# Optimization experiments

Hardware: AMD Instinct MI355X
Metric: run time of the kernel (lower is better)

## Reference

```python
import jax, jax.numpy as jnp
import numpy as np

K = 5        # spline kernel_size per dim (dim=2 -> 25 weight slots)
N = 60000    # input nodes
E = 360000   # input edges
N1 = 30000   # nodes after first graclus/max_pool
E2 = 180000  # edges of pooled graph
N2 = 15000   # nodes after second graclus pooling
G = 60       # graphs in batch


def _spline_basis(pseudo):
    """Open B-spline basis, degree 1, dim 2. pseudo: [E,2] in [0,1].
    Returns flat weight indices [E,4] and basis products [E,4]."""
    v = pseudo * (K - 1)
    i0 = jnp.clip(jnp.floor(v).astype(jnp.int32), 0, K - 1)   # [E,2]
    frac = v - jnp.floor(v)                                   # [E,2]
    idxs, ws = [], []
    for s0 in (0, 1):
        for s1 in (0, 1):
            ix = jnp.clip(i0[:, 0] + s0, 0, K - 1)
            iy = jnp.clip(i0[:, 1] + s1, 0, K - 1)
            w0 = frac[:, 0] if s0 else 1.0 - frac[:, 0]
            w1 = frac[:, 1] if s1 else 1.0 - frac[:, 1]
            idxs.append(ix + K * iy)
            ws.append(w0 * w1)
    return jnp.stack(idxs, -1), jnp.stack(ws, -1)


def _spline_conv(x, edge_index, pseudo, W, root, bias, num_nodes):
    """SplineConv: B-spline weighted messages, mean aggregation, root weight + bias."""
    src, dst = edge_index[0], edge_index[1]
    e = src.shape[0]
    idx, b = _spline_basis(pseudo)
    # dense per-edge basis over 25 kernel slots (only 4 nonzero per edge)
    B = jnp.zeros((e, K * K), x.dtype).at[jnp.arange(e)[:, None], idx].add(b)
    x_j = x[src]                                   # [E,Fin]
    fin, fout = W.shape[1], W.shape[2]
    xb = B[:, :, None] * x_j[:, None, :]           # [E,25,Fin]
    msg = xb.reshape(e, K * K * fin) @ W.reshape(K * K * fin, fout)
    agg = jax.ops.segment_sum(msg, dst, num_segments=num_nodes)
    cnt = jax.ops.segment_sum(jnp.ones((e,), x.dtype), dst, num_segments=num_nodes)
    agg = agg / jnp.maximum(cnt, 1.0)[:, None]     # mean aggregation
    return agg + x @ root + bias


def _seg_max_f(x, seg, n):
    m = jax.ops.segment_max(x, seg, num_segments=n)
    cnt = jax.ops.segment_sum(jnp.ones(seg.shape, x.dtype), seg, num_segments=n)
    return jnp.where((cnt > 0)[:, None], m, 0.0)


def _seg_max_i(x, seg, n):
    m = jax.ops.segment_max(x, seg, num_segments=n)
    return jnp.maximum(m, 0)


def _cartesian(pos, edge_index):
    # T.Cartesian(cat=False): attr = (pos[col]-pos[row]) / (2*max|.|) + 0.5
    cart = pos[edge_index[1]] - pos[edge_index[0]]
    scale = jnp.maximum(jnp.max(jnp.abs(cart)), 1e-12)
    return cart / (2.0 * scale) + 0.5


def setup_inputs():
    key = jax.random.key(0)
    ks = jax.random.split(key, 18)
    return {
        'x': jax.random.normal(ks[0], (N, 1), jnp.float32),
        'pos': jax.random.uniform(ks[1], (N, 2), jnp.float32),
        'edge_attr': jax.random.uniform(ks[2], (E, 2), jnp.float32),
        'edge_index': jax.random.randint(ks[3], (2, E), 0, N, jnp.int32),
        'batch': jnp.sort(jax.random.randint(ks[4], (N,), 0, G, jnp.int32)),
        'cluster1': jax.random.randint(ks[5], (N,), 0, N1, jnp.int32),
        'edge_index2': jax.random.randint(ks[6], (2, E2), 0, N1, jnp.int32),
        'cluster2': jax.random.randint(ks[7], (N1,), 0, N2, jnp.int32),
        'W1': jax.random.normal(ks[8], (K * K, 1, 32), jnp.float32) * 0.1,
        'root1': jax.random.normal(ks[9], (1, 32), jnp.float32) * 0.1,
        'bias1': jnp.zeros((32,), jnp.float32),
        'W2': jax.random.normal(ks[10], (K * K, 32, 64), jnp.float32) * 0.05,
        'root2': jax.random.normal(ks[11], (32, 64), jnp.float32) * 0.05,
        'bias2': jnp.zeros((64,), jnp.float32),
        'fc1_w': jax.random.normal(ks[12], (64, 128), jnp.float32) * 0.05,
        'fc1_b': jnp.zeros((128,), jnp.float32),
        'fc2_w': jax.random.normal(ks[13], (128, 3), jnp.float32) * 0.05,
        'fc2_b': jnp.zeros((3,), jnp.float32),
    }


def reference(x, pos, edge_attr, edge_index, batch, cluster1, edge_index2,
              cluster2, W1, root1, bias1, W2, root2, bias2,
              fc1_w, fc1_b, fc2_w, fc2_b):
    # conv1 + elu
    h = jax.nn.elu(_spline_conv(x, edge_index, edge_attr, W1, root1, bias1, N))
    # max_pool over graclus cluster1 (cluster given as input), Cartesian edge attrs
    x1 = _seg_max_f(h, cluster1, N1)
    pcnt = jax.ops.segment_sum(jnp.ones((N,), pos.dtype), cluster1, num_segments=N1)
    pos1 = jax.ops.segment_sum(pos, cluster1, num_segments=N1) / jnp.maximum(pcnt, 1.0)[:, None]
    batch1 = _seg_max_i(batch, cluster1, N1)
    attr2 = _cartesian(pos1, edge_index2)
    # conv2 + elu
    h2 = jax.nn.elu(_spline_conv(x1, edge_index2, attr2, W2, root2, bias2, N1))
    # max_pool_x over cluster2
    x2 = _seg_max_f(h2, cluster2, N2)
    batch2 = _seg_max_i(batch1, cluster2, N2)
    # global mean pool over graphs
    gsum = jax.ops.segment_sum(x2, batch2, num_segments=G)
    gcnt = jax.ops.segment_sum(jnp.ones((N2,), x2.dtype), batch2, num_segments=G)
    gm = gsum / jnp.maximum(gcnt, 1.0)[:, None]
    # head (dropout is identity in eval mode)
    h3 = jax.nn.elu(gm @ fc1_w + fc1_b)
    logits = h3 @ fc2_w + fc2_b
    return jax.nn.log_softmax(logits, axis=1)
```

## Files before the change

kernel.cpp:

```cpp
#include <hip/hip_runtime.h>
#include <math.h>

#define KD 5
#define NN 60000
#define EE 360000
#define NP1 30000
#define EE2 180000
#define NP2 15000
#define GG 60

#define FH 16
#define NBLK 512

#define PB2 120
#define CPB2 125


__device__ __forceinline__ unsigned fkey(float f) {
    unsigned u = __float_as_uint(f);
    return (u & 0x80000000u) ? ~u : (u | 0x80000000u);
}
__device__ __forceinline__ float fkey_inv(unsigned k) {
    unsigned u = (k & 0x80000000u) ? (k ^ 0x80000000u) : ~k;
    return __uint_as_float(u);
}

__device__ __forceinline__ void spline_basis(float p0, float p1, int* idx, float* w) {
    float v0 = p0 * 4.0f, v1 = p1 * 4.0f;
    float fl0 = floorf(v0), fl1 = floorf(v1);
    int i0 = min(max((int)fl0, 0), KD - 1);
    int i1 = min(max((int)fl1, 0), KD - 1);
    float fr0 = v0 - fl0, fr1 = v1 - fl1;
    int c = 0;
#pragma unroll
    for (int s0 = 0; s0 < 2; ++s0) {
#pragma unroll
        for (int s1 = 0; s1 < 2; ++s1) {
            int ix = min(i0 + s0, KD - 1);
            int iy = min(i1 + s1, KD - 1);
            float w0 = s0 ? fr0 : 1.0f - fr0;
            float w1 = s1 ? fr1 : 1.0f - fr1;
            idx[c] = ix + KD * iy;
            w[c] = w0 * w1;
            ++c;
        }
    }
}

__device__ __forceinline__ float elu1(float v) {
    return v > 0.0f ? v : expm1f(v);
}


__global__ void conv1_edge(const float* __restrict__ x, const float* __restrict__ ea,
                           const int* __restrict__ ei, const float* __restrict__ W1,
                           float* __restrict__ agg1, float* __restrict__ cnt1) {
    int gid = blockIdx.x * blockDim.x + threadIdx.x;
    if (gid >= EE * 32) return;
    int e = gid >> 5, f = gid & 31;
    int src = ei[e], dst = ei[EE + e];
    int idx[4]; float w[4];
    spline_basis(ea[2 * e], ea[2 * e + 1], idx, w);
    float coeff = 0.0f;
#pragma unroll
    for (int k = 0; k < 4; ++k) coeff += w[k] * W1[idx[k] * 32 + f];
    atomicAdd(&agg1[dst * 32 + f], x[src] * coeff);
    if (f == 0) atomicAdd(&cnt1[dst], 1.0f);
}

__global__ void conv1_fin(const float* __restrict__ x, const float* __restrict__ root1,
                          const float* __restrict__ bias1, const float* __restrict__ cnt1,
                          float* __restrict__ agg1) {
    int gid = blockIdx.x * blockDim.x + threadIdx.x;
    if (gid >= NN * 32) return;
    int n = gid >> 5, f = gid & 31;
    float v = agg1[gid] / fmaxf(cnt1[n], 1.0f) + x[n] * root1[f] + bias1[f];
    agg1[gid] = elu1(v);
}


__global__ void pool1(const float* __restrict__ h, const float* __restrict__ pos,
                      const int* __restrict__ batch, const int* __restrict__ cl1,
                      unsigned* __restrict__ x1key, int* __restrict__ ccnt1,
                      float* __restrict__ pos1, int* __restrict__ batch1) {
    int gid = blockIdx.x * blockDim.x + threadIdx.x;
    if (gid >= NN * 32) return;
    int n = gid >> 5, f = gid & 31;
    int c = cl1[n];
    atomicMax(&x1key[c * 32 + f], fkey(h[gid]));
    if (f == 0) {
        atomicAdd(&ccnt1[c], 1);
        atomicAdd(&pos1[c * 2], pos[n * 2]);
        atomicAdd(&pos1[c * 2 + 1], pos[n * 2 + 1]);
        atomicMax(&batch1[c], batch[n]);
    }
}

__global__ void pool1_fin(unsigned* __restrict__ x1key, const int* __restrict__ ccnt1,
                          float* __restrict__ pos1) {
    int gid = blockIdx.x * blockDim.x + threadIdx.x;
    if (gid >= NP1 * 32) return;
    int c = gid >> 5, f = gid & 31;
    int cnt = ccnt1[c];
    float v = cnt > 0 ? fkey_inv(x1key[gid]) : 0.0f;
    ((float*)x1key)[gid] = v;
    if (f < 2) pos1[c * 2 + f] = pos1[c * 2 + f] / fmaxf((float)cnt, 1.0f);
}


__global__ void cart_k(const float* __restrict__ pos1, const int* __restrict__ ei2,
                       float* __restrict__ attr2, unsigned* __restrict__ scaleb) {
    int e = blockIdx.x * blockDim.x + threadIdx.x;
    float m = 0.0f;
    if (e < EE2) {
        int s = ei2[e], d = ei2[EE2 + e];
        float c0 = pos1[d * 2] - pos1[s * 2];
        float c1 = pos1[d * 2 + 1] - pos1[s * 2 + 1];
        attr2[e * 2] = c0;
        attr2[e * 2 + 1] = c1;
        m = fmaxf(fabsf(c0), fabsf(c1));
    }
#pragma unroll
    for (int off = 32; off > 0; off >>= 1) m = fmaxf(m, __shfl_down(m, off));
    if ((threadIdx.x & 63) == 0) atomicMax(scaleb, __float_as_uint(m));
}

__global__ void attr2_fin(float* __restrict__ attr2, const unsigned* __restrict__ scaleb) {
    int gid = blockIdx.x * blockDim.x + threadIdx.x;
    if (gid >= EE2 * 2) return;
    float s = fmaxf(__uint_as_float(*scaleb), 1e-12f);
    attr2[gid] = attr2[gid] / (2.0f * s) + 0.5f;
}


__global__ __launch_bounds__(256) void conv2_lds(const float* __restrict__ x1,
                                                 const float* __restrict__ attr2,
                                                 const int* __restrict__ ei2,
                                                 const float* __restrict__ W2,
                                                 float* __restrict__ agg2,
                                                 float* __restrict__ cnt2) {
    __shared__ float wl[25 * 8 * FH * 4];
    const int q = blockIdx.x & 3;
    const int blk = blockIdx.x >> 2;
    const int t = threadIdx.x;

    for (int i = t; i < 25 * 8 * FH * 4; i += 256) {
        int c = i & 3;
        int fh = (i >> 2) & (FH - 1);
        int g = (i >> 6) & 7;
        int s = i >> 9;
        wl[i] = W2[s * 2048 + (g * 4 + c) * 64 + q * FH + fh];
    }
    __syncthreads();

    const int fh = t & (FH - 1);
    const int grp = t >> 4;
    const int EPB = (EE2 + NBLK - 1) / NBLK;
    const int e0 = blk * EPB;
    const int e_end = min(e0 + EPB, EE2);
    const float4* wl4 = (const float4*)wl;

    for (int e = e0 + grp; e < e_end; e += 16) {
        int src = ei2[e], dst = ei2[EE2 + e];
        int idx[4]; float w[4];
        spline_basis(attr2[2 * e], attr2[2 * e + 1], idx, w);
        const float4* xp = (const float4*)(x1 + src * 32);
        float4 xv[8];
#pragma unroll
        for (int g = 0; g < 8; ++g) xv[g] = xp[g];
        float msg = 0.0f;
#pragma unroll
        for (int k = 0; k < 4; ++k) {
            const float4* wp = wl4 + idx[k] * (8 * FH) + fh;
            float acc = 0.0f;
#pragma unroll
            for (int g = 0; g < 8; ++g) {
                float4 wv = wp[g * FH];
                acc += xv[g].x * wv.x;
                acc += xv[g].y * wv.y;
                acc += xv[g].z * wv.z;
                acc += xv[g].w * wv.w;
            }
            msg += w[k] * acc;
        }
        atomicAdd(&agg2[dst * 64 + q * FH + fh], msg);
        if (q == 0 && fh == 0) atomicAdd(&cnt2[dst], 1.0f);
    }
}

__global__ void conv2_fin(const float* __restrict__ x1, const float* __restrict__ root2,
                          const float* __restrict__ bias2, const float* __restrict__ cnt2,
                          float* __restrict__ agg2) {
    int gid = blockIdx.x * blockDim.x + threadIdx.x;
    if (gid >= NP1 * 64) return;
    int n = gid >> 6, f = gid & 63;
    float r = 0.0f;
    const float* xs = x1 + n * 32;
#pragma unroll
    for (int i = 0; i < 32; ++i) r += xs[i] * root2[i * 64 + f];
    float v = agg2[gid] / fmaxf(cnt2[n], 1.0f) + r + bias2[f];
    agg2[gid] = elu1(v);
}


__global__ void pool2(const float* __restrict__ h2, const int* __restrict__ batch1,
                      const int* __restrict__ cl2, unsigned* __restrict__ x2key,
                      int* __restrict__ ccnt2, int* __restrict__ batch2) {
    int gid = blockIdx.x * blockDim.x + threadIdx.x;
    if (gid >= NP1 * 64) return;
    int n = gid >> 6, f = gid & 63;
    int c = cl2[n];
    atomicMax(&x2key[c * 64 + f], fkey(h2[gid]));
    if (f == 0) {
        atomicAdd(&ccnt2[c], 1);
        atomicMax(&batch2[c], batch1[n]);
    }
}


__global__ __launch_bounds__(256) void pool2_part(const unsigned* __restrict__ x2key,
                                                  const int* __restrict__ ccnt2,
                                                  const int* __restrict__ batch2,
                                                  float* __restrict__ partial,
                                                  float* __restrict__ pcnt) {
    __shared__ float gs[GG * 64 + GG];
    const int t = threadIdx.x;
    for (int i = t; i < GG * 64 + GG; i += 256) gs[i] = 0.0f;
    __syncthreads();
    const int lane = t & 63, wv = t >> 6;
    const int c0 = blockIdx.x * CPB2;
    const int c1 = min(c0 + CPB2, NP2);
    for (int c = c0 + wv; c < c1; c += 4) {
        int cnt = ccnt2[c];
        int g = batch2[c];
        float v = cnt > 0 ? fkey_inv(x2key[c * 64 + lane]) : 0.0f;
        atomicAdd(&gs[g * 64 + lane], v);
        if (lane == 0) atomicAdd(&gs[GG * 64 + g], 1.0f);
    }
    __syncthreads();
    float* pb = partial + (size_t)blockIdx.x * (GG * 64);
    for (int i = t; i < GG * 64; i += 256) pb[i] = gs[i];
    if (t < GG) pcnt[blockIdx.x * GG + t] = gs[GG * 64 + t];
}


__global__ __launch_bounds__(128) void gpool_head(const float* __restrict__ partial,
                                                  const float* __restrict__ pcnt,
                                                  const float* __restrict__ fc1w,
                                                  const float* __restrict__ fc1b,
                                                  const float* __restrict__ fc2w,
                                                  const float* __restrict__ fc2b,
                                                  float* __restrict__ out) {
    const int g = blockIdx.x;
    const int t = threadIdx.x;
    __shared__ float red[128];
    __shared__ float acc2[128];
    __shared__ float gm[64];
    __shared__ float h3[128];
    __shared__ float lg[3];

    red[t] = (t < PB2) ? pcnt[t * GG + g] : 0.0f;
    __syncthreads();
    for (int s = 64; s > 0; s >>= 1) {
        if (t < s) red[t] += red[t + s];
        __syncthreads();
    }

    const int f = t & 63, h = t >> 6;
    float acc = 0.0f;
    for (int b = h * (PB2 / 2); b < (h + 1) * (PB2 / 2); ++b)
        acc += partial[(size_t)b * (GG * 64) + g * 64 + f];
    acc2[t] = acc;
    __syncthreads();
    if (t < 64) gm[t] = (acc2[t] + acc2[t + 64]) / fmaxf(red[0], 1.0f);
    __syncthreads();

    float a = fc1b[t];
#pragma unroll
    for (int i = 0; i < 64; ++i) a += gm[i] * fc1w[i * 128 + t];
    h3[t] = elu1(a);
    __syncthreads();
    if (t < 3) {
        float a2 = fc2b[t];
#pragma unroll
        for (int i = 0; i < 128; ++i) a2 += h3[i] * fc2w[i * 3 + t];
        lg[t] = a2;
    }
    __syncthreads();
    if (t == 0) {
        float m = fmaxf(lg[0], fmaxf(lg[1], lg[2]));
        float s = expf(lg[0] - m) + expf(lg[1] - m) + expf(lg[2] - m);
        float lse = m + logf(s);
        out[g * 3 + 0] = lg[0] - lse;
        out[g * 3 + 1] = lg[1] - lse;
        out[g * 3 + 2] = lg[2] - lse;
    }
}


extern "C" void kernel_launch(void* const* d_in, const int* in_sizes, int n_in,
                              void* d_out, int out_size, void* d_ws, size_t ws_size,
                              hipStream_t stream) {
    const float* x     = (const float*)d_in[0];
    const float* pos   = (const float*)d_in[1];
    const float* eattr = (const float*)d_in[2];
    const int*   ei    = (const int*)d_in[3];
    const int*   batch = (const int*)d_in[4];
    const int*   cl1   = (const int*)d_in[5];
    const int*   ei2   = (const int*)d_in[6];
    const int*   cl2   = (const int*)d_in[7];
    const float* W1    = (const float*)d_in[8];
    const float* root1 = (const float*)d_in[9];
    const float* bias1 = (const float*)d_in[10];
    const float* W2    = (const float*)d_in[11];
    const float* root2 = (const float*)d_in[12];
    const float* bias2 = (const float*)d_in[13];
    const float* fc1w  = (const float*)d_in[14];
    const float* fc1b  = (const float*)d_in[15];
    const float* fc2w  = (const float*)d_in[16];
    const float* fc2b  = (const float*)d_in[17];
    float* out = (float*)d_out;

    char* p = (char*)d_ws;
    auto carve = [&](size_t bytes) {
        char* r = p;
        p += (bytes + 255) & ~(size_t)255;
        return r;
    };
    float*    agg1    = (float*)carve((size_t)NN * 32 * 4);
    float*    cnt1    = (float*)carve((size_t)NN * 4);
    unsigned* x1key   = (unsigned*)carve((size_t)NP1 * 32 * 4);
    int*      ccnt1   = (int*)carve((size_t)NP1 * 4);
    float*    pos1    = (float*)carve((size_t)NP1 * 2 * 4);
    int*      batch1  = (int*)carve((size_t)NP1 * 4);
    unsigned* scaleb  = (unsigned*)carve(4);
    float*    attr2   = (float*)carve((size_t)EE2 * 2 * 4);
    float*    agg2    = (float*)carve((size_t)NP1 * 64 * 4);
    float*    cnt2    = (float*)carve((size_t)NP1 * 4);
    unsigned* x2key   = (unsigned*)carve((size_t)NP2 * 64 * 4);
    int*      ccnt2   = (int*)carve((size_t)NP2 * 4);
    int*      batch2  = (int*)carve((size_t)NP2 * 4);
    float*    partial = (float*)carve((size_t)PB2 * GG * 64 * 4);
    float*    pcnt    = (float*)carve((size_t)PB2 * GG * 4);
    size_t used = (size_t)(p - (char*)d_ws);
    hipMemsetAsync(d_ws, 0, used, stream);

    const int B = 256;
    conv1_edge<<<(EE * 32 + B - 1) / B, B, 0, stream>>>(x, eattr, ei, W1, agg1, cnt1);
    conv1_fin<<<(NN * 32 + B - 1) / B, B, 0, stream>>>(x, root1, bias1, cnt1, agg1);
    pool1<<<(NN * 32 + B - 1) / B, B, 0, stream>>>(agg1, pos, batch, cl1, x1key, ccnt1, pos1, batch1);
    pool1_fin<<<(NP1 * 32 + B - 1) / B, B, 0, stream>>>(x1key, ccnt1, pos1);
    cart_k<<<(EE2 + B - 1) / B, B, 0, stream>>>(pos1, ei2, attr2, scaleb);
    attr2_fin<<<(EE2 * 2 + B - 1) / B, B, 0, stream>>>(attr2, scaleb);
    conv2_lds<<<NBLK * 4, 256, 0, stream>>>((const float*)x1key, attr2, ei2, W2, agg2, cnt2);
    conv2_fin<<<(NP1 * 64 + B - 1) / B, B, 0, stream>>>((const float*)x1key, root2, bias2, cnt2, agg2);
    pool2<<<(NP1 * 64 + B - 1) / B, B, 0, stream>>>(agg2, batch1, cl2, x2key, ccnt2, batch2);
    pool2_part<<<PB2, 256, 0, stream>>>(x2key, ccnt2, batch2, partial, pcnt);
    gpool_head<<<GG, 128, 0, stream>>>(partial, pcnt, fc1w, fc1b, fc2w, fc2b, out);
}
```

Before: 278.5 us.

## Bucket conv2 edges by spline cell and keep cell weights in registers

Edges of the second spline conv are sorted into 25 buckets by their base spline cell, using a count/scan/scatter pass padded to wave multiples. Each wave then handles 64 edges that share one cell, so it loads the four needed W2 slices into registers once and computes all 64 output features per lane, with no LDS weight table. Degree counting moves into the Cartesian kernel and the separate normalisation kernel is folded into the basis computation. This adds three small kernels, a memset and a scatter pass. The bucket arrays reuse the agg1 buffer, and the 128 weight registers per thread may reduce occupancy.

Result: slower. 301.7 us (+8.3%).

```diff
diff --git a/kernel.cpp b/kernel.cpp
--- a/kernel.cpp
+++ b/kernel.cpp
@@ -9,8 +9,9 @@
 #define NP2 15000
 #define GG 60
 
-#define FH 16
-#define NBLK 512
+#define PADMAX (EE2 + 25 * 64)
+#define BWAVES ((PADMAX + 63) / 64)
+#define CBLK ((BWAVES + 3) / 4)
 
 #define PB2 120
 #define CPB2 125
@@ -47,6 +48,22 @@
     }
 }
 
+__device__ __forceinline__ void cell_basis(float c0, float c1, float s,
+                                           int& cell, float4& w4) {
+    float p0 = c0 / (2.0f * s) + 0.5f;
+    float p1 = c1 / (2.0f * s) + 0.5f;
+    float v0 = p0 * 4.0f, v1 = p1 * 4.0f;
+    float fl0 = floorf(v0), fl1 = floorf(v1);
+    int i0 = min(max((int)fl0, 0), KD - 1);
+    int i1 = min(max((int)fl1, 0), KD - 1);
+    float fr0 = v0 - fl0, fr1 = v1 - fl1;
+    cell = i0 + 5 * i1;
+    w4.x = (1.0f - fr0) * (1.0f - fr1);
+    w4.y = (1.0f - fr0) * fr1;
+    w4.z = fr0 * (1.0f - fr1);
+    w4.w = fr0 * fr1;
+}
+
 __device__ __forceinline__ float elu1(float v) {
     return v > 0.0f ? v : expm1f(v);
 }
@@ -109,82 +126,141 @@
 
 
 __global__ void cart_k(const float* __restrict__ pos1, const int* __restrict__ ei2,
-                       float* __restrict__ attr2, unsigned* __restrict__ scaleb) {
+                       float* __restrict__ cart, unsigned* __restrict__ scaleb,
+                       float* __restrict__ cnt2) {
     int e = blockIdx.x * blockDim.x + threadIdx.x;
     float m = 0.0f;
     if (e < EE2) {
         int s = ei2[e], d = ei2[EE2 + e];
         float c0 = pos1[d * 2] - pos1[s * 2];
         float c1 = pos1[d * 2 + 1] - pos1[s * 2 + 1];
-        attr2[e * 2] = c0;
-        attr2[e * 2 + 1] = c1;
+        cart[e * 2] = c0;
+        cart[e * 2 + 1] = c1;
         m = fmaxf(fabsf(c0), fabsf(c1));
+        atomicAdd(&cnt2[d], 1.0f);
     }
 #pragma unroll
     for (int off = 32; off > 0; off >>= 1) m = fmaxf(m, __shfl_down(m, off));
     if ((threadIdx.x & 63) == 0) atomicMax(scaleb, __float_as_uint(m));
 }
 
-__global__ void attr2_fin(float* __restrict__ attr2, const unsigned* __restrict__ scaleb) {
-    int gid = blockIdx.x * blockDim.x + threadIdx.x;
-    if (gid >= EE2 * 2) return;
-    float s = fmaxf(__uint_as_float(*scaleb), 1e-12f);
-    attr2[gid] = attr2[gid] / (2.0f * s) + 0.5f;
-}
-
-
-__global__ __launch_bounds__(256) void conv2_lds(const float* __restrict__ x1,
-                                                 const float* __restrict__ attr2,
-                                                 const int* __restrict__ ei2,
+
+__global__ void bucket_count(const float* __restrict__ cart,
+                             const unsigned* __restrict__ scaleb,
+                             int* __restrict__ ccount) {
+    __shared__ int lc[25];
+    int t = threadIdx.x;
+    if (t < 25) lc[t] = 0;
+    __syncthreads();
+    int e = blockIdx.x * blockDim.x + t;
+    if (e < EE2) {
+        float s = fmaxf(__uint_as_float(*scaleb), 1e-12f);
+        int cell; float4 w4;
+        cell_basis(cart[2 * e], cart[2 * e + 1], s, cell, w4);
+        atomicAdd(&lc[cell], 1);
+    }
+    __syncthreads();
+    if (t < 25 && lc[t] > 0) atomicAdd(&ccount[t], lc[t]);
+}
+
+__global__ void bucket_scan(const int* __restrict__ ccount, int* __restrict__ aoff,
+                            int* __restrict__ gcursor) {
+    if (blockIdx.x == 0 && threadIdx.x == 0) {
+        int acc = 0;
+        for (int c = 0; c < 25; ++c) {
+            aoff[c] = acc;
+            gcursor[c] = acc;
+            acc += (ccount[c] + 63) & ~63;
+        }
+        aoff[25] = acc;
+    }
+}
+
+__global__ void bucket_scatter(const float* __restrict__ cart,
+                               const unsigned* __restrict__ scaleb,
+                               const int* __restrict__ ei2,
+                               int* __restrict__ gcursor,
+                               int* __restrict__ bsrc, int* __restrict__ bdst,
+                               float4* __restrict__ bw) {
+    __shared__ int lc[25], lb[25];
+    int t = threadIdx.x;
+    if (t < 25) lc[t] = 0;
+    __syncthreads();
+    int e = blockIdx.x * blockDim.x + t;
+    bool valid = e < EE2;
+    int cell = 0, rank = 0;
+    float4 w4 = make_float4(0.f, 0.f, 0.f, 0.f);
+    if (valid) {
+        float s = fmaxf(__uint_as_float(*scaleb), 1e-12f);
+        cell_basis(cart[2 * e], cart[2 * e + 1], s, cell, w4);
+        rank = atomicAdd(&lc[cell], 1);
+    }
+    __syncthreads();
+    if (t < 25) lb[t] = lc[t] > 0 ? atomicAdd(&gcursor[t], lc[t]) : 0;
+    __syncthreads();
+    if (valid) {
+        int pos = lb[cell] + rank;
+        bsrc[pos] = ei2[e];
+        bdst[pos] = ei2[EE2 + e];
+        bw[pos] = w4;
+    }
+}
+
+
+__global__ __launch_bounds__(256) void conv2_reg(const int* __restrict__ bsrc,
+                                                 const int* __restrict__ bdst,
+                                                 const float4* __restrict__ bw,
+                                                 const int* __restrict__ aoff,
+                                                 const float* __restrict__ x1,
                                                  const float* __restrict__ W2,
-                                                 float* __restrict__ agg2,
-                                                 float* __restrict__ cnt2) {
-    __shared__ float wl[25 * 8 * FH * 4];
-    const int q = blockIdx.x & 3;
-    const int blk = blockIdx.x >> 2;
-    const int t = threadIdx.x;
-
-    for (int i = t; i < 25 * 8 * FH * 4; i += 256) {
-        int c = i & 3;
-        int fh = (i >> 2) & (FH - 1);
-        int g = (i >> 6) & 7;
-        int s = i >> 9;
-        wl[i] = W2[s * 2048 + (g * 4 + c) * 64 + q * FH + fh];
-    }
-    __syncthreads();
-
-    const int fh = t & (FH - 1);
-    const int grp = t >> 4;
-    const int EPB = (EE2 + NBLK - 1) / NBLK;
-    const int e0 = blk * EPB;
-    const int e_end = min(e0 + EPB, EE2);
-    const float4* wl4 = (const float4*)wl;
-
-    for (int e = e0 + grp; e < e_end; e += 16) {
-        int src = ei2[e], dst = ei2[EE2 + e];
-        int idx[4]; float w[4];
-        spline_basis(attr2[2 * e], attr2[2 * e + 1], idx, w);
+                                                 float* __restrict__ agg2) {
+    __shared__ int soff[26];
+    if (threadIdx.x < 26) soff[threadIdx.x] = aoff[threadIdx.x];
+    __syncthreads();
+    const int wave = (blockIdx.x << 2) + (threadIdx.x >> 6);
+    const int lane = threadIdx.x & 63;
+    const int base = wave << 6;
+    if (base >= soff[25]) return;
+    int cell = 0;
+#pragma unroll
+    for (int c = 1; c < 25; ++c)
+        if (base >= soff[c]) cell = c;
+    const int cx = cell % 5, cy = cell / 5;
+
+    float wreg[4][32];
+#pragma unroll
+    for (int k = 0; k < 4; ++k) {
+        int sl = min(cx + (k >> 1), 4) + 5 * min(cy + (k & 1), 4);
+        const float* wp = W2 + sl * 2048 + lane;
+#pragma unroll
+        for (int fi = 0; fi < 32; ++fi) wreg[k][fi] = wp[fi * 64];
+    }
+
+    for (int i = 0; i < 64; ++i) {
+        int e = base + i;
+        int src = bsrc[e];
+        if (src < 0) continue;
+        int dst = bdst[e];
+        float4 w4 = bw[e];
         const float4* xp = (const float4*)(x1 + src * 32);
         float4 xv[8];
 #pragma unroll
         for (int g = 0; g < 8; ++g) xv[g] = xp[g];
-        float msg = 0.0f;
+        float acc[4];
 #pragma unroll
         for (int k = 0; k < 4; ++k) {
-            const float4* wp = wl4 + idx[k] * (8 * FH) + fh;
-            float acc = 0.0f;
+            float a = 0.0f;
 #pragma unroll
             for (int g = 0; g < 8; ++g) {
-                float4 wv = wp[g * FH];
-                acc += xv[g].x * wv.x;
-                acc += xv[g].y * wv.y;
-                acc += xv[g].z * wv.z;
-                acc += xv[g].w * wv.w;
+                a += xv[g].x * wreg[k][g * 4 + 0];
+                a += xv[g].y * wreg[k][g * 4 + 1];
+                a += xv[g].z * wreg[k][g * 4 + 2];
+                a += xv[g].w * wreg[k][g * 4 + 3];
             }
-            msg += w[k] * acc;
+            acc[k] = a;
         }
-        atomicAdd(&agg2[dst * 64 + q * FH + fh], msg);
-        if (q == 0 && fh == 0) atomicAdd(&cnt2[dst], 1.0f);
+        float msg = w4.x * acc[0] + w4.y * acc[1] + w4.z * acc[2] + w4.w * acc[3];
+        atomicAdd(&agg2[dst * 64 + lane], msg);
     }
 }
 
@@ -334,7 +410,7 @@
     float*    pos1    = (float*)carve((size_t)NP1 * 2 * 4);
     int*      batch1  = (int*)carve((size_t)NP1 * 4);
     unsigned* scaleb  = (unsigned*)carve(4);
-    float*    attr2   = (float*)carve((size_t)EE2 * 2 * 4);
+    float*    cart    = (float*)carve((size_t)EE2 * 2 * 4);
     float*    agg2    = (float*)carve((size_t)NP1 * 64 * 4);
     float*    cnt2    = (float*)carve((size_t)NP1 * 4);
     unsigned* x2key   = (unsigned*)carve((size_t)NP2 * 64 * 4);
@@ -342,7 +418,15 @@
     int*      batch2  = (int*)carve((size_t)NP2 * 4);
     float*    partial = (float*)carve((size_t)PB2 * GG * 64 * 4);
     float*    pcnt    = (float*)carve((size_t)PB2 * GG * 4);
+    int*      ccount  = (int*)carve(25 * 4);
+    int*      aoff    = (int*)carve(26 * 4);
+    int*      gcursor = (int*)carve(25 * 4);
     size_t used = (size_t)(p - (char*)d_ws);
+
+    int*    bsrc = (int*)agg1;
+    int*    bdst = bsrc + PADMAX;
+    float4* bw   = (float4*)(bdst + PADMAX);
+
     hipMemsetAsync(d_ws, 0, used, stream);
 
     const int B = 256;
@@ -350,9 +434,12 @@
     conv1_fin<<<(NN * 32 + B - 1) / B, B, 0, stream>>>(x, root1, bias1, cnt1, agg1);
     pool1<<<(NN * 32 + B - 1) / B, B, 0, stream>>>(agg1, pos, batch, cl1, x1key, ccnt1, pos1, batch1);
     pool1_fin<<<(NP1 * 32 + B - 1) / B, B, 0, stream>>>(x1key, ccnt1, pos1);
-    cart_k<<<(EE2 + B - 1) / B, B, 0, stream>>>(pos1, ei2, attr2, scaleb);
-    attr2_fin<<<(EE2 * 2 + B - 1) / B, B, 0, stream>>>(attr2, scaleb);
-    conv2_lds<<<NBLK * 4, 256, 0, stream>>>((const float*)x1key, attr2, ei2, W2, agg2, cnt2);
+    hipMemsetAsync(bsrc, 0xFF, (size_t)PADMAX * 4, stream);
+    cart_k<<<(EE2 + B - 1) / B, B, 0, stream>>>(pos1, ei2, cart, scaleb, cnt2);
+    bucket_count<<<(EE2 + B - 1) / B, B, 0, stream>>>(cart, scaleb, ccount);
+    bucket_scan<<<1, 64, 0, stream>>>(ccount, aoff, gcursor);
+    bucket_scatter<<<(EE2 + B - 1) / B, B, 0, stream>>>(cart, scaleb, ei2, gcursor, bsrc, bdst, bw);
+    conv2_reg<<<CBLK, 256, 0, stream>>>(bsrc, bdst, bw, aoff, (const float*)x1key, W2, agg2);
     conv2_fin<<<(NP1 * 64 + B - 1) / B, B, 0, stream>>>((const float*)x1key, root2, bias2, cnt2, agg2);
     pool2<<<(NP1 * 64 + B - 1) / B, B, 0, stream>>>(agg2, batch1, cl2, x2key, ccnt2, batch2);
     pool2_part<<<PB2, 256, 0, stream>>>(x2key, ccnt2, batch2, partial, pcnt);
```

## Aggregate conv1 into 25 basis slots, then GEMM fused with pooling

Applied to the files above, without the earlier changes.

Conv1 now scatters each edge's basis-weighted scalar input into a per-node 25-slot accumulator instead of doing 32 per-feature atomics per edge. A new per-node kernel applies W1 to those 25 slots, adds root and bias, applies ELU and does the pool1 max directly. Conv2's finalize is also fused with pool2. The memset is limited to the buffers that actually need zeroing. This is meant to cut the atomic traffic in conv1 and remove intermediate round trips and launches, at the cost of a slightly different floating-point summation order.

New measurement: 301.5 us. 8.3% more time.

```diff
diff --git a/kernel.cpp b/kernel.cpp
--- a/kernel.cpp
+++ b/kernel.cpp
@@ -52,42 +52,43 @@
 }
 
 
-__global__ void conv1_edge(const float* __restrict__ x, const float* __restrict__ ea,
-                           const int* __restrict__ ei, const float* __restrict__ W1,
-                           float* __restrict__ agg1, float* __restrict__ cnt1) {
-    int gid = blockIdx.x * blockDim.x + threadIdx.x;
-    if (gid >= EE * 32) return;
-    int e = gid >> 5, f = gid & 31;
+__global__ void conv1_edge25(const float* __restrict__ x, const float* __restrict__ ea,
+                             const int* __restrict__ ei, float* __restrict__ agg25,
+                             float* __restrict__ cnt1) {
+    int e = blockIdx.x * blockDim.x + threadIdx.x;
+    if (e >= EE) return;
     int src = ei[e], dst = ei[EE + e];
     int idx[4]; float w[4];
     spline_basis(ea[2 * e], ea[2 * e + 1], idx, w);
-    float coeff = 0.0f;
-#pragma unroll
-    for (int k = 0; k < 4; ++k) coeff += w[k] * W1[idx[k] * 32 + f];
-    atomicAdd(&agg1[dst * 32 + f], x[src] * coeff);
-    if (f == 0) atomicAdd(&cnt1[dst], 1.0f);
-}
-
-__global__ void conv1_fin(const float* __restrict__ x, const float* __restrict__ root1,
-                          const float* __restrict__ bias1, const float* __restrict__ cnt1,
-                          float* __restrict__ agg1) {
-    int gid = blockIdx.x * blockDim.x + threadIdx.x;
-    if (gid >= NN * 32) return;
-    int n = gid >> 5, f = gid & 31;
-    float v = agg1[gid] / fmaxf(cnt1[n], 1.0f) + x[n] * root1[f] + bias1[f];
-    agg1[gid] = elu1(v);
-}
-
-
-__global__ void pool1(const float* __restrict__ h, const float* __restrict__ pos,
-                      const int* __restrict__ batch, const int* __restrict__ cl1,
-                      unsigned* __restrict__ x1key, int* __restrict__ ccnt1,
-                      float* __restrict__ pos1, int* __restrict__ batch1) {
-    int gid = blockIdx.x * blockDim.x + threadIdx.x;
-    if (gid >= NN * 32) return;
-    int n = gid >> 5, f = gid & 31;
+    float xs = x[src];
+#pragma unroll
+    for (int k = 0; k < 4; ++k) atomicAdd(&agg25[dst * 25 + idx[k]], w[k] * xs);
+    atomicAdd(&cnt1[dst], 1.0f);
+}
+
+
+__global__ __launch_bounds__(256) void conv1gemm_pool1(
+        const float* __restrict__ x, const float* __restrict__ W1,
+        const float* __restrict__ root1, const float* __restrict__ bias1,
+        const float* __restrict__ cnt1, const float* __restrict__ agg25,
+        const float* __restrict__ pos, const int* __restrict__ batch,
+        const int* __restrict__ cl1, unsigned* __restrict__ x1key,
+        int* __restrict__ ccnt1, float* __restrict__ pos1,
+        int* __restrict__ batch1) {
+    __shared__ float a25[8][25];
+    const int nb = blockIdx.x * 8;
+    const int t = threadIdx.x;
+    for (int i = t; i < 8 * 25; i += 256)
+        a25[i / 25][i % 25] = agg25[nb * 25 + i];
+    __syncthreads();
+    const int nn = t >> 5, f = t & 31;
+    const int n = nb + nn;
+    float dot = 0.0f;
+#pragma unroll
+    for (int s = 0; s < 25; ++s) dot += a25[nn][s] * W1[s * 32 + f];
+    float v = elu1(dot / fmaxf(cnt1[n], 1.0f) + x[n] * root1[f] + bias1[f]);
     int c = cl1[n];
-    atomicMax(&x1key[c * 32 + f], fkey(h[gid]));
+    atomicMax(&x1key[c * 32 + f], fkey(v));
     if (f == 0) {
         atomicAdd(&ccnt1[c], 1);
         atomicAdd(&pos1[c * 2], pos[n * 2]);
@@ -188,9 +189,12 @@
     }
 }
 
-__global__ void conv2_fin(const float* __restrict__ x1, const float* __restrict__ root2,
-                          const float* __restrict__ bias2, const float* __restrict__ cnt2,
-                          float* __restrict__ agg2) {
+
+__global__ void conv2fin_pool2(const float* __restrict__ x1, const float* __restrict__ root2,
+                               const float* __restrict__ bias2, const float* __restrict__ cnt2,
+                               const float* __restrict__ agg2, const int* __restrict__ cl2,
+                               const int* __restrict__ batch1, unsigned* __restrict__ x2key,
+                               int* __restrict__ ccnt2, int* __restrict__ batch2) {
     int gid = blockIdx.x * blockDim.x + threadIdx.x;
     if (gid >= NP1 * 64) return;
     int n = gid >> 6, f = gid & 63;
@@ -198,19 +202,9 @@
     const float* xs = x1 + n * 32;
 #pragma unroll
     for (int i = 0; i < 32; ++i) r += xs[i] * root2[i * 64 + f];
-    float v = agg2[gid] / fmaxf(cnt2[n], 1.0f) + r + bias2[f];
-    agg2[gid] = elu1(v);
-}
-
-
-__global__ void pool2(const float* __restrict__ h2, const int* __restrict__ batch1,
-                      const int* __restrict__ cl2, unsigned* __restrict__ x2key,
-                      int* __restrict__ ccnt2, int* __restrict__ batch2) {
-    int gid = blockIdx.x * blockDim.x + threadIdx.x;
-    if (gid >= NP1 * 64) return;
-    int n = gid >> 6, f = gid & 63;
+    float v = elu1(agg2[gid] / fmaxf(cnt2[n], 1.0f) + r + bias2[f]);
     int c = cl2[n];
-    atomicMax(&x2key[c * 64 + f], fkey(h2[gid]));
+    atomicMax(&x2key[c * 64 + f], fkey(v));
     if (f == 0) {
         atomicAdd(&ccnt2[c], 1);
         atomicMax(&batch2[c], batch1[n]);
@@ -327,34 +321,36 @@
         p += (bytes + 255) & ~(size_t)255;
         return r;
     };
-    float*    agg1    = (float*)carve((size_t)NN * 32 * 4);
+    float*    agg25   = (float*)carve((size_t)NN * 25 * 4);
     float*    cnt1    = (float*)carve((size_t)NN * 4);
     unsigned* x1key   = (unsigned*)carve((size_t)NP1 * 32 * 4);
     int*      ccnt1   = (int*)carve((size_t)NP1 * 4);
     float*    pos1    = (float*)carve((size_t)NP1 * 2 * 4);
     int*      batch1  = (int*)carve((size_t)NP1 * 4);
     unsigned* scaleb  = (unsigned*)carve(4);
-    float*    attr2   = (float*)carve((size_t)EE2 * 2 * 4);
     float*    agg2    = (float*)carve((size_t)NP1 * 64 * 4);
     float*    cnt2    = (float*)carve((size_t)NP1 * 4);
     unsigned* x2key   = (unsigned*)carve((size_t)NP2 * 64 * 4);
     int*      ccnt2   = (int*)carve((size_t)NP2 * 4);
     int*      batch2  = (int*)carve((size_t)NP2 * 4);
+    size_t zero_bytes = (size_t)(p - (char*)d_ws);
+    float*    attr2   = (float*)carve((size_t)EE2 * 2 * 4);
     float*    partial = (float*)carve((size_t)PB2 * GG * 64 * 4);
     float*    pcnt    = (float*)carve((size_t)PB2 * GG * 4);
-    size_t used = (size_t)(p - (char*)d_ws);
-    hipMemsetAsync(d_ws, 0, used, stream);
+
+    hipMemsetAsync(d_ws, 0, zero_bytes, stream);
 
     const int B = 256;
-    conv1_edge<<<(EE * 32 + B - 1) / B, B, 0, stream>>>(x, eattr, ei, W1, agg1, cnt1);
-    conv1_fin<<<(NN * 32 + B - 1) / B, B, 0, stream>>>(x, root1, bias1, cnt1, agg1);
-    pool1<<<(NN * 32 + B - 1) / B, B, 0, stream>>>(agg1, pos, batch, cl1, x1key, ccnt1, pos1, batch1);
+    conv1_edge25<<<(EE + B - 1) / B, B, 0, stream>>>(x, eattr, ei, agg25, cnt1);
+    conv1gemm_pool1<<<NN / 8, B, 0, stream>>>(x, W1, root1, bias1, cnt1, agg25,
+                                              pos, batch, cl1, x1key, ccnt1, pos1, batch1);
     pool1_fin<<<(NP1 * 32 + B - 1) / B, B, 0, stream>>>(x1key, ccnt1, pos1);
     cart_k<<<(EE2 + B - 1) / B, B, 0, stream>>>(pos1, ei2, attr2, scaleb);
     attr2_fin<<<(EE2 * 2 + B - 1) / B, B, 0, stream>>>(attr2, scaleb);
-    conv2_lds<<<NBLK * 4, 256, 0, stream>>>((const float*)x1key, attr2, ei2, W2, agg2, cnt2);
-    conv2_fin<<<(NP1 * 64 + B - 1) / B, B, 0, stream>>>((const float*)x1key, root2, bias2, cnt2, agg2);
-    pool2<<<(NP1 * 64 + B - 1) / B, B, 0, stream>>>(agg2, batch1, cl2, x2key, ccnt2, batch2);
-    pool2_part<<<PB2, 256, 0, stream>>>(x2key, ccnt2, batch2, partial, pcnt);
+    conv2_lds<<<NBLK * 4, B, 0, stream>>>((const float*)x1key, attr2, ei2, W2, agg2, cnt2);
+    conv2fin_pool2<<<(NP1 * 64 + B - 1) / B, B, 0, stream>>>((const float*)x1key, root2, bias2,
+                                                             cnt2, agg2, cl2, batch1, x2key,
+                                                             ccnt2, batch2);
+    pool2_part<<<PB2, B, 0, stream>>>(x2key, ccnt2, batch2, partial, pcnt);
     gpool_head<<<GG, 128, 0, stream>>>(partial, pcnt, fc1w, fc1b, fc2w, fc2b, out);
 }
```
